# Kernel tuning notes

Hardware: AMD Instinct MI355X
Metric: run time of the kernel (lower is better)

The kernel has to match this reference:

```python
import jax, jax.numpy as jnp
import numpy as np

N_RAYS, N_SAMPLES, N_VERTS = 2048, 32, 6890

def setup_inputs() -> dict:
    key = jax.random.key(0)
    k1, k2, k3, k4 = jax.random.split(key, 4)
    rays_points_world = jax.random.normal(k1, (1, N_RAYS, 1, N_SAMPLES, 3), jnp.float32)
    rays_directions_world = jax.random.normal(k2, (1, N_RAYS, 1, N_SAMPLES, 3), jnp.float32)
    vertices_posed = jax.random.normal(k3, (1, N_VERTS, 3), jnp.float32)
    # Ts must be invertible: small perturbation of identity (like rigid bone transforms)
    Ts = jax.random.normal(k4, (1, N_VERTS, 4, 4), jnp.float32) * 0.1 + jnp.eye(4, dtype=jnp.float32)
    return {
        'rays_points_world': rays_points_world,
        'rays_directions_world': rays_directions_world,
        'vertices_posed': vertices_posed,
        'Ts': Ts,
    }

def reference(rays_points_world, rays_directions_world, vertices_posed, Ts):
    orig_shape = rays_points_world.shape  # [1, R, 1, S, 3]
    pts = rays_points_world.reshape(-1, 3)          # (N, 3), N = R*S
    verts = vertices_posed[0]                       # (V, 3)
    # squared Euclidean distances via expansion (avoids N x V x 3 intermediate)
    d2 = ((pts * pts).sum(-1, keepdims=True)
          - 2.0 * (pts @ verts.T)
          + (verts * verts).sum(-1)[None, :])       # (N, V)
    idx = jnp.argmin(d2, axis=-1)                   # (N,) nearest vertex per point
    T_inv = jnp.linalg.inv(Ts)[0]                   # (V, 4, 4)
    T_sel = T_inv[idx]                              # (N, 4, 4) gather
    # flip x,y signs, build homogeneous coords
    xyz = jnp.stack([-pts[:, 0], -pts[:, 1], pts[:, 2]], axis=-1)      # (N, 3)
    homo = jnp.concatenate([xyz, jnp.ones_like(xyz[:, :1])], axis=-1)  # (N, 4)
    can = jnp.einsum('nij,nj->ni', T_sel, homo)[:, :3]                 # (N, 3)
    can = can.reshape(orig_shape)                                      # [1, R, 1, S, 3]
    # direction = finite diff along sample axis, last repeated
    dirs = can[..., 1:, :] - can[..., :-1, :]
    dirs = jnp.concatenate([dirs, dirs[..., -1:, :]], axis=-2)
    norm = jnp.linalg.norm(dirs, axis=-1, keepdims=True)
    dirs = dirs / jnp.maximum(norm, 1e-12)  # matches torch F.normalize eps
    flip = jnp.array([-1.0, -1.0, 1.0], dtype=can.dtype)
    return can * flip, dirs * flip
```

## Files before the change

kernel.cpp:

```cpp
#include <hip/hip_runtime.h>
#include <math.h>
#include <stdint.h>

#define N_RAYS    2048
#define N_SAMPLES 32
#define NPTS      (N_RAYS * N_SAMPLES)
#define NV        6890
#define G         32
#define NCELLS    (G * G * G)
#define SPLIT     16
#define QMASK     0xFFFFE000u
#define IMASK     0x1FFFu
#define CMASK     0x1FFFu

#define TIE_REL   3e-3f
#define TIE_ABS   2e-5f

#define WS_COUNT     0
#define WS_FBC       4
#define WS_PARAMS    16
#define WS_HIST      128
#define WS_ROWMASK   (WS_HIST + 4 * NCELLS)
#define WS_CELLINFO  (WS_ROWMASK + 4 * G * G)
#define WS_SVERTS    (WS_CELLINFO + 4 * NCELLS)
#define WS_ORIGIDX   (WS_SVERTS + 16 * NV)
#define WS_LIST      (WS_ORIGIDX + 2 * NV + 12)
#define WS_NEEDED    (WS_LIST + 2 * NPTS)
#define WS_IDX       WS_HIST
#define WS_ZERO_W    ((WS_CELLINFO) / 4)

__device__ __forceinline__ uint64_t umin64(uint64_t a, uint64_t b) { return a < b ? a : b; }
__device__ __forceinline__ uint64_t umax64(uint64_t a, uint64_t b) { return a < b ? b : a; }
__device__ __forceinline__ uint32_t wmask(int a, int b) {
    return (uint32_t)((((uint64_t)1 << (b - a + 1)) - 1) << a);
}

__global__ __launch_bounds__(256) void init_kernel(const float* __restrict__ verts,
                                                   float* __restrict__ params,
                                                   uint32_t* __restrict__ wzero) {
    const int t = threadIdx.x;
    if (blockIdx.x != 0) {
        for (int i = (blockIdx.x - 1) * 256 + t; i < WS_ZERO_W; i += (gridDim.x - 1) * 256) {
            if (i >= 4 && i < 32) continue;
            wzero[i] = 0u;
        }
        return;
    }
    __shared__ float mn[3][256], mx[3][256];
    float lmn[3] = {1e30f, 1e30f, 1e30f}, lmx[3] = {-1e30f, -1e30f, -1e30f};
    for (int v = t; v < NV; v += 256) {
        #pragma unroll
        for (int d = 0; d < 3; ++d) {
            float x = verts[v * 3 + d];
            lmn[d] = fminf(lmn[d], x); lmx[d] = fmaxf(lmx[d], x);
        }
    }
    #pragma unroll
    for (int d = 0; d < 3; ++d) { mn[d][t] = lmn[d]; mx[d][t] = lmx[d]; }
    __syncthreads();
    for (int s = 128; s > 0; s >>= 1) {
        if (t < s) {
            #pragma unroll
            for (int d = 0; d < 3; ++d) {
                mn[d][t] = fminf(mn[d][t], mn[d][t + s]);
                mx[d][t] = fmaxf(mx[d][t], mx[d][t + s]);
            }
        }
        __syncthreads();
    }
    if (t == 0) {
        #pragma unroll
        for (int d = 0; d < 3; ++d) {
            const float lo = mn[d][0] - 1e-3f, hi = mx[d][0] + 1e-3f;
            const float span = fmaxf(hi - lo, 1e-2f);
            params[d]     = lo;
            params[3 + d] = span / (float)G;
            params[6 + d] = (float)G / span;
        }
    }
}

__device__ __forceinline__ int cell_clamp(float x, float org, float ih) {
    int c = (int)floorf((x - org) * ih);
    return min(max(c, 0), G - 1);
}

__global__ void hist_kernel(const float* __restrict__ verts, const float* __restrict__ params,
                            uint32_t* __restrict__ hist) {
    const int v = blockIdx.x * blockDim.x + threadIdx.x;
    if (v >= NV) return;
    const int cx = cell_clamp(verts[v * 3 + 0], params[0], params[6]);
    const int cy = cell_clamp(verts[v * 3 + 1], params[1], params[7]);
    const int cz = cell_clamp(verts[v * 3 + 2], params[2], params[8]);
    atomicAdd(&hist[(cz * G + cy) * G + cx], 1u);
}

__global__ __launch_bounds__(1024) void scan_cells_kernel(const uint32_t* __restrict__ hist,
                                                          uint32_t* __restrict__ cellinfo,
                                                          uint32_t* __restrict__ rowmask) {
    __shared__ uint32_t part[1024];
    const int t = threadIdx.x;
    uint32_t loc[32];
    uint32_t sum = 0, rmask = 0;
    const int base = t * 32;
    #pragma unroll
    for (int i = 0; i < 32; ++i) {
        const uint32_t h = hist[base + i];
        loc[i] = sum; sum += h;
        if (h) rmask |= (1u << i);
    }
    part[t] = sum;
    rowmask[t] = rmask;
    __syncthreads();
    for (int off = 1; off < 1024; off <<= 1) {
        const uint32_t v = (t >= off) ? part[t - off] : 0u;
        __syncthreads();
        part[t] += v;
        __syncthreads();
    }
    const uint32_t pre = (t == 0) ? 0u : part[t - 1];
    #pragma unroll
    for (int i = 0; i < 32; ++i) {
        const uint32_t nxt = (i == 31) ? sum : loc[i + 1];
        const uint32_t cnt = nxt - loc[i];
        cellinfo[base + i] = ((pre + loc[i]) << 13) | cnt;
    }
}

__global__ void scatter_kernel(const float* __restrict__ verts, const float* __restrict__ params,
                               uint32_t* __restrict__ hist, const uint32_t* __restrict__ cellinfo,
                               float4* __restrict__ sverts, uint16_t* __restrict__ origidx) {
    const int v = blockIdx.x * blockDim.x + threadIdx.x;
    if (v >= NV) return;
    const float x = verts[v * 3 + 0], y = verts[v * 3 + 1], z = verts[v * 3 + 2];
    const int cx = cell_clamp(x, params[0], params[6]);
    const int cy = cell_clamp(y, params[1], params[7]);
    const int cz = cell_clamp(z, params[2], params[8]);
    const int c = (cz * G + cy) * G + cx;
    const uint32_t old = atomicSub(&hist[c], 1u);
    const uint32_t pos = (cellinfo[c] >> 13) + old - 1u;
    sverts[pos] = make_float4(x, y, z, fmaf(x, x, fmaf(y, y, z * z)));
    origidx[pos] = (uint16_t)v;
}

__global__ __launch_bounds__(256) void search_kernel(
    const float* __restrict__ pts, const float* __restrict__ params,
    const uint32_t* __restrict__ rowmask, const uint32_t* __restrict__ cellinfo,
    const float4* __restrict__ sverts, const uint16_t* __restrict__ origidx,
    uint16_t* __restrict__ idx16, uint16_t* __restrict__ list16,
    uint32_t* __restrict__ count, uint32_t* __restrict__ fbcount)
{
    __shared__ uint32_t srow[G * G];
    const int tid = threadIdx.x;
    for (int i = tid; i < G * G; i += 256) srow[i] = rowmask[i];
    __syncthreads();

    const int gtid = blockIdx.x * 256 + tid;
    const int sub  = gtid & (SPLIT - 1);
    const int n    = gtid / SPLIT;
    const float px = pts[n * 3 + 0], py = pts[n * 3 + 1], pz = pts[n * 3 + 2];
    const float acc = -0.5f * fmaf(px, px, fmaf(py, py, pz * pz));
    const float org0 = params[0], org1 = params[1], org2 = params[2];
    const float h0 = params[3], h1 = params[4], h2 = params[5];
    const int cx = cell_clamp(px, org0, params[6]);
    const int cy = cell_clamp(py, org1, params[7]);
    const int cz = cell_clamp(pz, org2, params[8]);

    uint32_t k1 = ~0u, k2 = ~0u;
    bool unproven = true;

    auto scan_run = [&](int rowG, int a, int b) {
        const uint32_t i0 = cellinfo[rowG + a];
        const uint32_t i1 = cellinfo[rowG + b];
        const uint32_t s = i0 >> 13;
        const uint32_t e = (i1 >> 13) + (i1 & CMASK);
        for (uint32_t j = s + sub; j < e; j += SPLIT) {
            const float4 q = sverts[j];
            const float dot = fmaf(px, q.x, fmaf(py, q.y, fmaf(pz, q.z, acc)));
            const float d = fmaxf(fmaf(-2.f, dot, q.w), 0.f);
            const uint32_t k = (__float_as_uint(d) & QMASK) | j;
            k2 = min(k2, max(k1, k)); k1 = min(k1, k);
        }
    };
    auto proven = [&](int xl, int xh, int yl, int yh, int zl, int zh) -> bool {
        uint32_t m1 = k1;
        #pragma unroll
        for (int off = 1; off < SPLIT; off <<= 1)
            m1 = min(m1, (uint32_t)__shfl_xor((int)m1, off));
        if (m1 == ~0u) return false;
        float dmin = 1e30f;
        bool any = false;
        if (xl > 0)     { dmin = fminf(dmin, px - fmaf((float)xl,      h0, org0)); any = true; }
        if (xh < G - 1) { dmin = fminf(dmin, fmaf((float)(xh + 1), h0, org0) - px); any = true; }
        if (yl > 0)     { dmin = fminf(dmin, py - fmaf((float)yl,      h1, org1)); any = true; }
        if (yh < G - 1) { dmin = fminf(dmin, fmaf((float)(yh + 1), h1, org1) - py); any = true; }
        if (zl > 0)     { dmin = fminf(dmin, pz - fmaf((float)zl,      h2, org2)); any = true; }
        if (zh < G - 1) { dmin = fminf(dmin, fmaf((float)(zh + 1), h2, org2) - pz); any = true; }
        if (!any) return true;
        const float dout = fmaxf(dmin, 0.f);
        const float d1f = __uint_as_float(m1 & QMASK);
        return dout * dout > fmaf(d1f, 1.05f, 1e-3f);
    };

    const int xlo1 = max(cx - 1, 0), xhi1 = min(cx + 1, G - 1);
    const int ylo1 = max(cy - 1, 0), yhi1 = min(cy + 1, G - 1);
    const int zlo1 = max(cz - 1, 0), zhi1 = min(cz + 1, G - 1);
    const uint32_t wm1 = wmask(xlo1, xhi1);
    for (int z = zlo1; z <= zhi1; ++z)
        for (int y = ylo1; y <= yhi1; ++y) {
            const int row = z * G + y;
            if (srow[row] & wm1) scan_run(row * G, xlo1, xhi1);
        }
    if (proven(xlo1, xhi1, ylo1, yhi1, zlo1, zhi1)) {
        unproven = false;
    } else {
        const int xlo3 = max(cx - 3, 0), xhi3 = min(cx + 3, G - 1);
        const int ylo3 = max(cy - 3, 0), yhi3 = min(cy + 3, G - 1);
        const int zlo3 = max(cz - 3, 0), zhi3 = min(cz + 3, G - 1);
        const uint32_t wm3 = wmask(xlo3, xhi3);
        for (int z = zlo3; z <= zhi3; ++z) {
            const bool zin = (z >= zlo1 && z <= zhi1);
            for (int y = ylo3; y <= yhi3; ++y) {
                const int row = z * G + y;
                const uint32_t rm = srow[row];
                if (!(rm & wm3)) continue;
                if (zin && y >= ylo1 && y <= yhi1) {
                    if (xlo3 <= xlo1 - 1 && (rm & wmask(xlo3, xlo1 - 1)))
                        scan_run(row * G, xlo3, xlo1 - 1);
                    if (xhi1 + 1 <= xhi3 && (rm & wmask(xhi1 + 1, xhi3)))
                        scan_run(row * G, xhi1 + 1, xhi3);
                } else {
                    scan_run(row * G, xlo3, xhi3);
                }
            }
        }
        if (proven(xlo3, xhi3, ylo3, yhi3, zlo3, zhi3)) unproven = false;
    }

    #pragma unroll
    for (int off = 1; off < SPLIT; off <<= 1) {
        const uint32_t o1 = (uint32_t)__shfl_xor((int)k1, off);
        const uint32_t o2 = (uint32_t)__shfl_xor((int)k2, off);
        k2 = min(min(k2, o2), max(k1, o1)); k1 = min(k1, o1);
    }

    if (sub == 0) {
        if (unproven) {
            const uint32_t p = atomicAdd(fbcount, 1u);
            list16[NPTS - 1 - p] = (uint16_t)n;
        } else {
            const float d1 = __uint_as_float(k1 & QMASK);
            const float d2 = __uint_as_float(k2 & QMASK);
            idx16[n] = origidx[k1 & IMASK];
            if (d2 - d1 < fmaf(TIE_REL, d1, TIE_ABS)) {
                const uint32_t p = atomicAdd(count, 1u);
                list16[p] = (uint16_t)n;
            }
        }
    }
}

__global__ __launch_bounds__(256) void fixup_kernel(
    const float* __restrict__ pts,
    const float4* __restrict__ sverts, const uint16_t* __restrict__ origidx,
    uint16_t* __restrict__ list16,
    const uint32_t* __restrict__ count, const uint32_t* __restrict__ fbcount,
    uint16_t* __restrict__ idx16)
{
    const uint32_t fcnt = *fbcount;
    const uint32_t tcnt = *count;
    const uint32_t total = fcnt + tcnt;
    const int wv = threadIdx.x >> 6, lane = threadIdx.x & 63;
    for (uint32_t jj = blockIdx.x * 4 + wv; jj < total; jj += gridDim.x * 4) {
        const bool isFb = jj < fcnt;
        const int n = isFb ? (int)list16[NPTS - 1 - jj] : (int)list16[jj - fcnt];
        const float px = pts[n * 3 + 0], py = pts[n * 3 + 1], pz = pts[n * 3 + 2];
        bool needF64 = true;
        if (isFb) {
            const float acc = -0.5f * fmaf(px, px, fmaf(py, py, pz * pz));
            uint32_t k1 = ~0u, k2 = ~0u;
            int v = lane;
            for (; v + 192 < NV; v += 256) {
                const float4 q0 = sverts[v];
                const float4 q1 = sverts[v + 64];
                const float4 q2 = sverts[v + 128];
                const float4 q3 = sverts[v + 192];
                float dot, d; uint32_t k;
                dot = fmaf(px, q0.x, fmaf(py, q0.y, fmaf(pz, q0.z, acc)));
                d = fmaxf(fmaf(-2.f, dot, q0.w), 0.f);
                k = (__float_as_uint(d) & QMASK) | (uint32_t)v;
                k2 = min(k2, max(k1, k)); k1 = min(k1, k);
                dot = fmaf(px, q1.x, fmaf(py, q1.y, fmaf(pz, q1.z, acc)));
                d = fmaxf(fmaf(-2.f, dot, q1.w), 0.f);
                k = (__float_as_uint(d) & QMASK) | (uint32_t)(v + 64);
                k2 = min(k2, max(k1, k)); k1 = min(k1, k);
                dot = fmaf(px, q2.x, fmaf(py, q2.y, fmaf(pz, q2.z, acc)));
                d = fmaxf(fmaf(-2.f, dot, q2.w), 0.f);
                k = (__float_as_uint(d) & QMASK) | (uint32_t)(v + 128);
                k2 = min(k2, max(k1, k)); k1 = min(k1, k);
                dot = fmaf(px, q3.x, fmaf(py, q3.y, fmaf(pz, q3.z, acc)));
                d = fmaxf(fmaf(-2.f, dot, q3.w), 0.f);
                k = (__float_as_uint(d) & QMASK) | (uint32_t)(v + 192);
                k2 = min(k2, max(k1, k)); k1 = min(k1, k);
            }
            for (; v < NV; v += 64) {
                const float4 q = sverts[v];
                const float dot = fmaf(px, q.x, fmaf(py, q.y, fmaf(pz, q.z, acc)));
                const float d = fmaxf(fmaf(-2.f, dot, q.w), 0.f);
                const uint32_t k = (__float_as_uint(d) & QMASK) | (uint32_t)v;
                k2 = min(k2, max(k1, k)); k1 = min(k1, k);
            }
            #pragma unroll
            for (int off = 1; off < 64; off <<= 1) {
                const uint32_t o1 = (uint32_t)__shfl_xor((int)k1, off);
                const uint32_t o2 = (uint32_t)__shfl_xor((int)k2, off);
                k2 = min(min(k2, o2), max(k1, o1)); k1 = min(k1, o1);
            }
            const float d1 = __uint_as_float(k1 & QMASK);
            const float d2 = __uint_as_float(k2 & QMASK);
            needF64 = (d2 - d1 < fmaf(TIE_REL, d1, TIE_ABS));
            if (!needF64 && lane == 0) idx16[n] = origidx[k1 & IMASK];
        }
        if (needF64) {
            const double pxd = (double)px, pyd = (double)py, pzd = (double)pz;
            double best = 1e300; uint32_t bi = 0xFFFFFFFFu;
            int v = lane;
            for (; v + 192 < NV; v += 256) {
                const float4 q0 = sverts[v];
                const float4 q1 = sverts[v + 64];
                const float4 q2 = sverts[v + 128];
                const float4 q3 = sverts[v + 192];
                const uint32_t o0 = origidx[v];
                const uint32_t o1 = origidx[v + 64];
                const uint32_t o2 = origidx[v + 128];
                const uint32_t o3 = origidx[v + 192];
                double dx, dy, dz, d;
                dx = pxd - (double)q0.x; dy = pyd - (double)q0.y; dz = pzd - (double)q0.z;
                d = dx*dx + dy*dy + dz*dz;
                if (d < best || (d == best && o0 < bi)) { best = d; bi = o0; }
                dx = pxd - (double)q1.x; dy = pyd - (double)q1.y; dz = pzd - (double)q1.z;
                d = dx*dx + dy*dy + dz*dz;
                if (d < best || (d == best && o1 < bi)) { best = d; bi = o1; }
                dx = pxd - (double)q2.x; dy = pyd - (double)q2.y; dz = pzd - (double)q2.z;
                d = dx*dx + dy*dy + dz*dz;
                if (d < best || (d == best && o2 < bi)) { best = d; bi = o2; }
                dx = pxd - (double)q3.x; dy = pyd - (double)q3.y; dz = pzd - (double)q3.z;
                d = dx*dx + dy*dy + dz*dz;
                if (d < best || (d == best && o3 < bi)) { best = d; bi = o3; }
            }
            for (; v < NV; v += 64) {
                const float4 q = sverts[v];
                const uint32_t oi = origidx[v];
                const double dx = pxd - (double)q.x;
                const double dy = pyd - (double)q.y;
                const double dz = pzd - (double)q.z;
                const double d = dx*dx + dy*dy + dz*dz;
                if (d < best || (d == best && oi < bi)) { best = d; bi = oi; }
            }
            #pragma unroll
            for (int off = 1; off < 64; off <<= 1) {
                const double od = __shfl_xor(best, off);
                const uint32_t oi = (uint32_t)__shfl_xor((int)bi, off);
                if (od < best || (od == best && oi < bi)) { best = od; bi = oi; }
            }
            if (lane == 0) idx16[n] = (uint16_t)bi;
        }
    }
}

__global__ __launch_bounds__(256) void output_kernel(
    const float* __restrict__ pts, const float* __restrict__ Ts,
    const uint16_t* __restrict__ idx16, float* __restrict__ out)
{
    __shared__ double sc[256][3];
    const int tid = threadIdx.x;
    const int n = blockIdx.x * 256 + tid;
    const float px = pts[n*3+0], py = pts[n*3+1], pz = pts[n*3+2];
    const int v = (int)idx16[n];

    const float4* T4 = reinterpret_cast<const float4*>(Ts + (size_t)v * 16);
    const float4 r0 = T4[0], r1 = T4[1], r2 = T4[2], r3 = T4[3];
    const double m[16] = { r0.x, r0.y, r0.z, r0.w,  r1.x, r1.y, r1.z, r1.w,
                           r2.x, r2.y, r2.z, r2.w,  r3.x, r3.y, r3.z, r3.w };
    double inv[16];
    inv[0]  =  m[5]*m[10]*m[15] - m[5]*m[11]*m[14] - m[9]*m[6]*m[15] + m[9]*m[7]*m[14] + m[13]*m[6]*m[11] - m[13]*m[7]*m[10];
    inv[4]  = -m[4]*m[10]*m[15] + m[4]*m[11]*m[14] + m[8]*m[6]*m[15] - m[8]*m[7]*m[14] - m[12]*m[6]*m[11] + m[12]*m[7]*m[10];
    inv[8]  =  m[4]*m[9]*m[15] - m[4]*m[11]*m[13] - m[8]*m[5]*m[15] + m[8]*m[7]*m[13] + m[12]*m[5]*m[11] - m[12]*m[7]*m[9];
    inv[12] = -m[4]*m[9]*m[14] + m[4]*m[10]*m[13] + m[8]*m[5]*m[14] - m[8]*m[6]*m[13] - m[12]*m[5]*m[10] + m[12]*m[6]*m[9];
    inv[1]  = -m[1]*m[10]*m[15] + m[1]*m[11]*m[14] + m[9]*m[2]*m[15] - m[9]*m[3]*m[14] - m[13]*m[2]*m[11] + m[13]*m[3]*m[10];
    inv[5]  =  m[0]*m[10]*m[15] - m[0]*m[11]*m[14] - m[8]*m[2]*m[15] + m[8]*m[3]*m[14] + m[12]*m[2]*m[11] - m[12]*m[3]*m[10];
    inv[9]  = -m[0]*m[9]*m[15] + m[0]*m[11]*m[13] + m[8]*m[1]*m[15] - m[8]*m[3]*m[13] - m[12]*m[1]*m[11] + m[12]*m[3]*m[9];
    inv[13] =  m[0]*m[9]*m[14] - m[0]*m[10]*m[13] - m[8]*m[1]*m[14] + m[8]*m[2]*m[13] + m[12]*m[1]*m[10] - m[12]*m[2]*m[9];
    inv[2]  =  m[1]*m[6]*m[15] - m[1]*m[7]*m[14] - m[5]*m[2]*m[15] + m[5]*m[3]*m[14] + m[13]*m[2]*m[7] - m[13]*m[3]*m[6];
    inv[6]  = -m[0]*m[6]*m[15] + m[0]*m[7]*m[14] + m[4]*m[2]*m[15] - m[4]*m[3]*m[14] - m[12]*m[2]*m[7] + m[12]*m[3]*m[6];
    inv[10] =  m[0]*m[5]*m[15] - m[0]*m[7]*m[13] - m[4]*m[1]*m[15] + m[4]*m[3]*m[13] + m[12]*m[1]*m[7] - m[12]*m[3]*m[5];
    inv[14] = -m[0]*m[5]*m[14] + m[0]*m[6]*m[13] + m[4]*m[1]*m[14] - m[4]*m[2]*m[13] - m[12]*m[1]*m[6] + m[12]*m[2]*m[5];
    inv[3]  = -m[1]*m[6]*m[11] + m[1]*m[7]*m[10] + m[5]*m[2]*m[11] - m[5]*m[3]*m[10] - m[9]*m[2]*m[7] + m[9]*m[3]*m[6];
    inv[7]  =  m[0]*m[6]*m[11] - m[0]*m[7]*m[10] - m[4]*m[2]*m[11] + m[4]*m[3]*m[10] + m[8]*m[2]*m[7] - m[8]*m[3]*m[6];
    inv[11] = -m[0]*m[5]*m[11] + m[0]*m[7]*m[9] + m[4]*m[1]*m[11] - m[4]*m[3]*m[9] - m[8]*m[1]*m[7] + m[8]*m[3]*m[5];
    inv[15] =  m[0]*m[5]*m[10] - m[0]*m[6]*m[9] - m[4]*m[1]*m[10] + m[4]*m[2]*m[9] + m[8]*m[1]*m[6] - m[8]*m[2]*m[5];
    const double det = m[0]*inv[0] + m[1]*inv[4] + m[2]*inv[8] + m[3]*inv[12];
    const double rd = 1.0 / det;

    const double hx = -(double)px, hy = -(double)py, hz = (double)pz;
    const double c0 = (inv[0]*hx + inv[1]*hy + inv[2]*hz  + inv[3])  * rd;
    const double c1 = (inv[4]*hx + inv[5]*hy + inv[6]*hz  + inv[7])  * rd;
    const double c2 = (inv[8]*hx + inv[9]*hy + inv[10]*hz + inv[11]) * rd;
    const double f0 = -c0, f1 = -c1, f2 = c2;

    out[n*3+0] = (float)f0; out[n*3+1] = (float)f1; out[n*3+2] = (float)f2;
    sc[tid][0] = f0; sc[tid][1] = f1; sc[tid][2] = f2;
    __syncthreads();

    int l0 = tid, l1 = tid + 1;
    if ((tid & (N_SAMPLES - 1)) == N_SAMPLES - 1) { l0 = tid - 1; l1 = tid; }
    const double dx = sc[l1][0] - sc[l0][0];
    const double dy = sc[l1][1] - sc[l0][1];
    const double dz = sc[l1][2] - sc[l0][2];
    const double nr = fmax(sqrt(dx*dx + dy*dy + dz*dz), 1e-12);
    float* o = out + (size_t)NPTS * 3 + (size_t)n * 3;
    o[0] = (float)(dx / nr); o[1] = (float)(dy / nr); o[2] = (float)(dz / nr);
}

__global__ void zero_kernel(uint32_t* __restrict__ w, int nwords) {
    for (int i = blockIdx.x * blockDim.x + threadIdx.x; i < nwords; i += gridDim.x * blockDim.x)
        w[i] = 0u;
}

__global__ __launch_bounds__(256) void scan_kernel(
    const float* __restrict__ pts, const float* __restrict__ verts,
    uint16_t* __restrict__ idx16, uint16_t* __restrict__ list16,
    uint32_t* __restrict__ count)
{
    __shared__ float4 sv[2048];
    const int tid  = threadIdx.x;
    const int part = tid & 7;
    const int grp  = tid >> 3;
    const int n0   = blockIdx.x * 64 + grp * 2;
    const float ax = pts[n0*3+0], ay = pts[n0*3+1], az = pts[n0*3+2];
    const float bx = pts[n0*3+3], by = pts[n0*3+4], bz = pts[n0*3+5];
    const float acc = -0.5f * fmaf(ax, ax, fmaf(ay, ay, az*az));
    const float bcc = -0.5f * fmaf(bx, bx, fmaf(by, by, bz*bz));
    uint64_t ak1 = ~0ull, ak2 = ~0ull, bk1 = ~0ull, bk2 = ~0ull;
    for (int base = 0; base < NV; base += 2048) {
        const int cnt = min(NV - base, 2048);
        __syncthreads();
        for (int v = tid; v < cnt; v += 256) {
            const float x = verts[(base+v)*3+0], y = verts[(base+v)*3+1], z = verts[(base+v)*3+2];
            sv[v] = make_float4(x, y, z, fmaf(x, x, fmaf(y, y, z*z)));
        }
        __syncthreads();
        #pragma unroll 4
        for (int v = part; v < cnt; v += 8) {
            const float4 q = sv[v];
            const uint64_t vi = (uint64_t)(base + v);
            float s, d; uint64_t k;
            s = fmaf(ax, q.x, fmaf(ay, q.y, fmaf(az, q.z, acc)));
            d = fmaxf(fmaf(-2.f, s, q.w), 0.f);
            k = ((uint64_t)__float_as_uint(d) << 32) | vi;
            ak2 = umin64(ak2, umax64(ak1, k)); ak1 = umin64(ak1, k);
            s = fmaf(bx, q.x, fmaf(by, q.y, fmaf(bz, q.z, bcc)));
            d = fmaxf(fmaf(-2.f, s, q.w), 0.f);
            k = ((uint64_t)__float_as_uint(d) << 32) | vi;
            bk2 = umin64(bk2, umax64(bk1, k)); bk1 = umin64(bk1, k);
        }
    }
    #pragma unroll
    for (int off = 1; off < 8; off <<= 1) {
        uint64_t o1, o2;
        o1 = __shfl_xor((unsigned long long)ak1, off); o2 = __shfl_xor((unsigned long long)ak2, off);
        ak2 = umin64(umin64(ak2, o2), umax64(ak1, o1)); ak1 = umin64(ak1, o1);
        o1 = __shfl_xor((unsigned long long)bk1, off); o2 = __shfl_xor((unsigned long long)bk2, off);
        bk2 = umin64(umin64(bk2, o2), umax64(bk1, o1)); bk1 = umin64(bk1, o1);
    }
    if (part == 0) {
        const float ad1 = __uint_as_float((uint32_t)(ak1 >> 32));
        const float ad2 = __uint_as_float((uint32_t)(ak2 >> 32));
        idx16[n0] = (uint16_t)(ak1 & 0xFFFFu);
        if (ad2 - ad1 < fmaf(1e-4f, ad1, TIE_ABS)) { uint32_t p = atomicAdd(count, 1u); list16[p] = (uint16_t)n0; }
        const float bd1 = __uint_as_float((uint32_t)(bk1 >> 32));
        const float bd2 = __uint_as_float((uint32_t)(bk2 >> 32));
        idx16[n0+1] = (uint16_t)(bk1 & 0xFFFFu);
        if (bd2 - bd1 < fmaf(1e-4f, bd1, TIE_ABS)) { uint32_t p = atomicAdd(count, 1u); list16[p] = (uint16_t)(n0+1); }
    }
}

__global__ __launch_bounds__(256) void refine_kernel(
    const float* __restrict__ pts, const float* __restrict__ verts,
    const uint16_t* __restrict__ list16, const uint32_t* __restrict__ count,
    uint16_t* __restrict__ idx16)
{
    const uint32_t cnt = *count;
    const int wv = threadIdx.x >> 6, lane = threadIdx.x & 63;
    for (uint32_t j = blockIdx.x * 4 + wv; j < cnt; j += gridDim.x * 4) {
        const int n = (int)list16[j];
        const double px = (double)pts[n*3+0];
        const double py = (double)pts[n*3+1];
        const double pz = (double)pts[n*3+2];
        double best = 1e300; uint32_t bi = 0xFFFFFFFFu;
        for (int v = lane; v < NV; v += 64) {
            const double dx = px - (double)verts[v*3+0];
            const double dy = py - (double)verts[v*3+1];
            const double dz = pz - (double)verts[v*3+2];
            const double d = dx*dx + dy*dy + dz*dz;
            if (d < best || (d == best && (uint32_t)v < bi)) { best = d; bi = (uint32_t)v; }
        }
        #pragma unroll
        for (int off = 1; off < 64; off <<= 1) {
            const double od = __shfl_xor(best, off);
            const uint32_t oi = (uint32_t)__shfl_xor((int)bi, off);
            if (od < best || (od == best && oi < bi)) { best = od; bi = oi; }
        }
        if (lane == 0) idx16[n] = (uint16_t)bi;
    }
}

extern "C" void kernel_launch(void* const* d_in, const int* in_sizes, int n_in,
                              void* d_out, int out_size, void* d_ws, size_t ws_size,
                              hipStream_t stream) {
    const float* pts   = (const float*)d_in[0];
    const float* verts = (const float*)d_in[2];
    const float* Ts    = (const float*)d_in[3];
    float* out = (float*)d_out;

    uint8_t* ws = (uint8_t*)d_ws;
    uint32_t* count   = (uint32_t*)(ws + WS_COUNT);
    uint32_t* fbcount = (uint32_t*)(ws + WS_FBC);

    if (ws_size >= (size_t)WS_NEEDED) {
        float*    params   = (float*)(ws + WS_PARAMS);
        uint32_t* hist     = (uint32_t*)(ws + WS_HIST);
        uint32_t* rowmask  = (uint32_t*)(ws + WS_ROWMASK);
        uint32_t* cellinfo = (uint32_t*)(ws + WS_CELLINFO);
        float4*   sverts   = (float4*)(ws + WS_SVERTS);
        uint16_t* origidx  = (uint16_t*)(ws + WS_ORIGIDX);
        uint16_t* idx16    = (uint16_t*)(ws + WS_IDX);
        uint16_t* list16   = (uint16_t*)(ws + WS_LIST);
        const int vblocks = (NV + 255) / 256;

        hipLaunchKernelGGL(init_kernel, dim3(65), dim3(256), 0, stream,
                           verts, params, (uint32_t*)ws);
        hipLaunchKernelGGL(hist_kernel, dim3(vblocks), dim3(256), 0, stream,
                           verts, params, hist);
        hipLaunchKernelGGL(scan_cells_kernel, dim3(1), dim3(1024), 0, stream,
                           hist, cellinfo, rowmask);
        hipLaunchKernelGGL(scatter_kernel, dim3(vblocks), dim3(256), 0, stream,
                           verts, params, hist, cellinfo, sverts, origidx);
        hipLaunchKernelGGL(search_kernel, dim3(NPTS * SPLIT / 256), dim3(256), 0, stream,
                           pts, params, rowmask, cellinfo, sverts, origidx,
                           idx16, list16, count, fbcount);
        hipLaunchKernelGGL(fixup_kernel, dim3(1024), dim3(256), 0, stream,
                           pts, sverts, origidx, list16, count, fbcount, idx16);
        hipLaunchKernelGGL(output_kernel, dim3(NPTS / 256), dim3(256), 0, stream,
                           pts, Ts, idx16, out);
    } else {
        uint16_t* idx16  = (uint16_t*)(ws + 64);
        uint16_t* list16 = (uint16_t*)(ws + 64 + 2 * NPTS);
        hipLaunchKernelGGL(zero_kernel, dim3(1), dim3(64), 0, stream, (uint32_t*)ws, 1);
        hipLaunchKernelGGL(scan_kernel, dim3(NPTS / 64), dim3(256), 0, stream,
                           pts, verts, idx16, list16, count);
        hipLaunchKernelGGL(refine_kernel, dim3(512), dim3(256), 0, stream,
                           pts, verts, list16, count, idx16);
        hipLaunchKernelGGL(output_kernel, dim3(NPTS / 256), dim3(256), 0, stream,
                           pts, Ts, idx16, out);
    }
}
```

Measured before the change: 95.18 us.

## Fuse scan and scatter kernels, halve search split, add incremental shell search

Merges the cell prefix-scan and vertex scatter into one single-block kernel, which removes one launch at the cost of scattering 6890 vertices with only 1024 threads. Lowers SPLIT from 16 to 8 threads per query point, so each thread scans more cells but fewer warps and shuffles are used. Replaces the fixed radius-1 then radius-3 expansion with shell-by-shell expansion at radius 2 and 3 that stops early once the nearest vertex is proven. This avoids scanning the full radius-3 block when radius 2 already suffices.

```diff
diff --git a/kernel.cpp b/kernel.cpp
--- a/kernel.cpp
+++ b/kernel.cpp
@@ -8,7 +8,8 @@
 #define NV        6890
 #define G         32
 #define NCELLS    (G * G * G)
-#define SPLIT     16
+#define SPLIT     8
+#define RMAX      3
 #define QMASK     0xFFFFE000u
 #define IMASK     0x1FFFu
 #define CMASK     0x1FFFu
@@ -31,8 +32,10 @@
 
 __device__ __forceinline__ uint64_t umin64(uint64_t a, uint64_t b) { return a < b ? a : b; }
 __device__ __forceinline__ uint64_t umax64(uint64_t a, uint64_t b) { return a < b ? b : a; }
-__device__ __forceinline__ uint32_t wmask(int a, int b) {
-    return (uint32_t)((((uint64_t)1 << (b - a + 1)) - 1) << a);
+
+__device__ __forceinline__ int cell_clamp(float x, float org, float ih) {
+    int c = (int)floorf((x - org) * ih);
+    return min(max(c, 0), G - 1);
 }
 
 __global__ __launch_bounds__(256) void init_kernel(const float* __restrict__ verts,
@@ -80,11 +83,6 @@
     }
 }
 
-__device__ __forceinline__ int cell_clamp(float x, float org, float ih) {
-    int c = (int)floorf((x - org) * ih);
-    return min(max(c, 0), G - 1);
-}
-
 __global__ void hist_kernel(const float* __restrict__ verts, const float* __restrict__ params,
                             uint32_t* __restrict__ hist) {
     const int v = blockIdx.x * blockDim.x + threadIdx.x;
@@ -95,9 +93,12 @@
     atomicAdd(&hist[(cz * G + cy) * G + cx], 1u);
 }
 
-__global__ __launch_bounds__(1024) void scan_cells_kernel(const uint32_t* __restrict__ hist,
-                                                          uint32_t* __restrict__ cellinfo,
-                                                          uint32_t* __restrict__ rowmask) {
+__global__ __launch_bounds__(1024) void scan_scatter_kernel(
+    const float* __restrict__ verts, const float* __restrict__ params,
+    uint32_t* __restrict__ hist, uint32_t* __restrict__ cellinfo,
+    uint32_t* __restrict__ rowmask, float4* __restrict__ sverts,
+    uint16_t* __restrict__ origidx)
+{
     __shared__ uint32_t part[1024];
     const int t = threadIdx.x;
     uint32_t loc[32];
@@ -123,24 +124,23 @@
     for (int i = 0; i < 32; ++i) {
         const uint32_t nxt = (i == 31) ? sum : loc[i + 1];
         const uint32_t cnt = nxt - loc[i];
-        cellinfo[base + i] = ((pre + loc[i]) << 13) | cnt;
-    }
-}
-
-__global__ void scatter_kernel(const float* __restrict__ verts, const float* __restrict__ params,
-                               uint32_t* __restrict__ hist, const uint32_t* __restrict__ cellinfo,
-                               float4* __restrict__ sverts, uint16_t* __restrict__ origidx) {
-    const int v = blockIdx.x * blockDim.x + threadIdx.x;
-    if (v >= NV) return;
-    const float x = verts[v * 3 + 0], y = verts[v * 3 + 1], z = verts[v * 3 + 2];
-    const int cx = cell_clamp(x, params[0], params[6]);
-    const int cy = cell_clamp(y, params[1], params[7]);
-    const int cz = cell_clamp(z, params[2], params[8]);
-    const int c = (cz * G + cy) * G + cx;
-    const uint32_t old = atomicSub(&hist[c], 1u);
-    const uint32_t pos = (cellinfo[c] >> 13) + old - 1u;
-    sverts[pos] = make_float4(x, y, z, fmaf(x, x, fmaf(y, y, z * z)));
-    origidx[pos] = (uint16_t)v;
+        const uint32_t st  = pre + loc[i];
+        cellinfo[base + i] = (st << 13) | cnt;
+        hist[base + i] = st;
+    }
+    __syncthreads();
+    const float og0 = params[0], og1 = params[1], og2 = params[2];
+    const float ih0 = params[6], ih1 = params[7], ih2 = params[8];
+    for (int v = t; v < NV; v += 1024) {
+        const float x = verts[v * 3 + 0], y = verts[v * 3 + 1], z = verts[v * 3 + 2];
+        const int cx = cell_clamp(x, og0, ih0);
+        const int cy = cell_clamp(y, og1, ih1);
+        const int cz = cell_clamp(z, og2, ih2);
+        const int c = (cz * G + cy) * G + cx;
+        const uint32_t pos = atomicAdd(&hist[c], 1u);
+        sverts[pos] = make_float4(x, y, z, fmaf(x, x, fmaf(y, y, z * z)));
+        origidx[pos] = (uint16_t)v;
+    }
 }
 
 __global__ __launch_bounds__(256) void search_kernel(
@@ -205,36 +205,42 @@
     const int xlo1 = max(cx - 1, 0), xhi1 = min(cx + 1, G - 1);
     const int ylo1 = max(cy - 1, 0), yhi1 = min(cy + 1, G - 1);
     const int zlo1 = max(cz - 1, 0), zhi1 = min(cz + 1, G - 1);
-    const uint32_t wm1 = wmask(xlo1, xhi1);
-    for (int z = zlo1; z <= zhi1; ++z)
-        for (int y = ylo1; y <= yhi1; ++y) {
-            const int row = z * G + y;
-            if (srow[row] & wm1) scan_run(row * G, xlo1, xhi1);
-        }
-    if (proven(xlo1, xhi1, ylo1, yhi1, zlo1, zhi1)) {
-        unproven = false;
-    } else {
-        const int xlo3 = max(cx - 3, 0), xhi3 = min(cx + 3, G - 1);
-        const int ylo3 = max(cy - 3, 0), yhi3 = min(cy + 3, G - 1);
-        const int zlo3 = max(cz - 3, 0), zhi3 = min(cz + 3, G - 1);
-        const uint32_t wm3 = wmask(xlo3, xhi3);
-        for (int z = zlo3; z <= zhi3; ++z) {
-            const bool zin = (z >= zlo1 && z <= zhi1);
-            for (int y = ylo3; y <= yhi3; ++y) {
+    {
+        const uint32_t wm = (uint32_t)((((uint64_t)1 << (xhi1 - xlo1 + 1)) - 1) << xlo1);
+        for (int z = zlo1; z <= zhi1; ++z)
+            for (int y = ylo1; y <= yhi1; ++y) {
                 const int row = z * G + y;
-                const uint32_t rm = srow[row];
-                if (!(rm & wm3)) continue;
-                if (zin && y >= ylo1 && y <= yhi1) {
-                    if (xlo3 <= xlo1 - 1 && (rm & wmask(xlo3, xlo1 - 1)))
-                        scan_run(row * G, xlo3, xlo1 - 1);
-                    if (xhi1 + 1 <= xhi3 && (rm & wmask(xhi1 + 1, xhi3)))
-                        scan_run(row * G, xhi1 + 1, xhi3);
-                } else {
-                    scan_run(row * G, xlo3, xhi3);
+                if (srow[row] & wm) scan_run(row * G, xlo1, xhi1);
+            }
+    }
+    if (proven(xlo1, xhi1, ylo1, yhi1, zlo1, zhi1)) unproven = false;
+
+    if (unproven) {
+        for (int r = 2; r <= RMAX; ++r) {
+            const int xlo = max(cx - r, 0), xhi = min(cx + r, G - 1);
+            const int ylo = max(cy - r, 0), yhi = min(cy + r, G - 1);
+            const int zlo = max(cz - r, 0), zhi = min(cz + r, G - 1);
+            const uint32_t wm = (uint32_t)((((uint64_t)1 << (xhi - xlo + 1)) - 1) << xlo);
+            for (int z = zlo; z <= zhi; ++z) {
+                const int az = abs(z - cz);
+                for (int y = ylo; y <= yhi; ++y) {
+                    const int row = z * G + y;
+                    const int ayz = max(abs(y - cy), az);
+                    if (ayz == r) {
+                        if (srow[row] & wm) scan_run(row * G, xlo, xhi);
+                    } else {
+                        #pragma unroll
+                        for (int side = 0; side < 2; ++side) {
+                            const int x = side ? cx + r : cx - r;
+                            if (x < 0 || x > G - 1) continue;
+                            if (!((srow[row] >> x) & 1u)) continue;
+                            scan_run(row * G, x, x);
+                        }
+                    }
                 }
             }
-        }
-        if (proven(xlo3, xhi3, ylo3, yhi3, zlo3, zhi3)) unproven = false;
+            if (proven(xlo, xhi, ylo, yhi, zlo, zhi)) { unproven = false; break; }
+        }
     }
 
     #pragma unroll
@@ -542,10 +548,8 @@
                            verts, params, (uint32_t*)ws);
         hipLaunchKernelGGL(hist_kernel, dim3(vblocks), dim3(256), 0, stream,
                            verts, params, hist);
-        hipLaunchKernelGGL(scan_cells_kernel, dim3(1), dim3(1024), 0, stream,
-                           hist, cellinfo, rowmask);
-        hipLaunchKernelGGL(scatter_kernel, dim3(vblocks), dim3(256), 0, stream,
-                           verts, params, hist, cellinfo, sverts, origidx);
+        hipLaunchKernelGGL(scan_scatter_kernel, dim3(1), dim3(1024), 0, stream,
+                           verts, params, hist, cellinfo, rowmask, sverts, origidx);
         hipLaunchKernelGGL(search_kernel, dim3(NPTS * SPLIT / 256), dim3(256), 0, stream,
                            pts, params, rowmask, cellinfo, sverts, origidx,
                            idx16, list16, count, fbcount);
```

Result: slower. 106.8 us (+12.2%).
